# Kernel tuning notes

Measured on AMD Instinct MI355X. Metric: run time of the kernel, lower is better.

The kernel has to match this reference:

```python
import jax, jax.numpy as jnp
import numpy as np

NT, NRV, NR = 100000, 200000, 300000  # tile / road_vertex / road node counts
E = 400000                             # edges per edge type
B, H, P, A = 64, 128, 64, 512          # graphs, hidden, player_state_dim, action_dim


def _gat(h_src, h_dst, src, dst, W, a_s, a_d, b, n_dst):
    # PyG GATConv, heads=1, shared lin for src/dst, no self loops (bipartite)
    hs = h_src @ W                      # [Ns, H]
    hd = h_dst @ W                      # [Nd, H]
    e = jax.nn.leaky_relu((hs @ a_s)[src] + (hd @ a_d)[dst], 0.2)  # [E]
    m = jax.ops.segment_max(e, dst, num_segments=n_dst)
    w = jnp.exp(e - m[dst])
    denom = jax.ops.segment_sum(w, dst, num_segments=n_dst)
    alpha = w / jnp.maximum(denom[dst], 1e-16)                      # segment softmax
    out = jax.ops.segment_sum(alpha[:, None] * hs[src], dst, num_segments=n_dst)
    return out + b


def _mean_pool(x, batch, nb):
    s = jax.ops.segment_sum(x, batch, num_segments=nb)
    c = jax.ops.segment_sum(jnp.ones((x.shape[0],), x.dtype), batch, num_segments=nb)
    return s / jnp.maximum(c, 1.0)[:, None]


def setup_inputs():
    ks = iter(jax.random.split(jax.random.key(0), 64))
    f32 = jnp.float32

    def lin(i, o):
        return (jax.random.normal(next(ks), (i, o), f32) / np.float32(np.sqrt(i)))

    d = {}
    d['x_tile'] = jax.random.normal(next(ks), (NT, 8), f32)
    d['x_rv'] = jax.random.normal(next(ks), (NRV, 13), f32)
    d['x_road'] = jax.random.normal(next(ks), (NR, 4), f32)
    d['x_player'] = jax.random.normal(next(ks), (B, P), f32)
    # node encoders
    d['enc_t_W'] = lin(8, H);  d['enc_t_b'] = jnp.zeros((H,), f32)
    d['enc_rv_W'] = lin(13, H); d['enc_rv_b'] = jnp.zeros((H,), f32)
    d['enc_r_W'] = lin(4, H);  d['enc_r_b'] = jnp.zeros((H,), f32)
    # six GAT convs
    for name in ['rv2t', 't2rv', 'r2rv', 'rv2r', 't2r', 'r2t']:
        d[name + '_W'] = lin(H, H)
        d[name + '_as'] = jax.random.normal(next(ks), (H,), f32) * 0.1
        d[name + '_ad'] = jax.random.normal(next(ks), (H,), f32) * 0.1
        d[name + '_b'] = jnp.zeros((H,), f32)
    # player MLP + output head (input: 3H pooled + H player)
    d['fc1_W'] = lin(P, H); d['fc1_b'] = jnp.zeros((H,), f32)
    d['fc2_W'] = lin(H, H); d['fc2_b'] = jnp.zeros((H,), f32)
    d['out_W'] = lin(4 * H, A); d['out_b'] = jnp.zeros((A,), f32)
    # edges (src bounded by source-type count, dst by dest-type count)
    ri = lambda n, hi: jax.random.randint(n, (E,), 0, hi, jnp.int32)
    d['e_rv2t_src'] = ri(next(ks), NRV); d['e_rv2t_dst'] = ri(next(ks), NT)
    d['e_t2rv_src'] = ri(next(ks), NT);  d['e_t2rv_dst'] = ri(next(ks), NRV)
    d['e_r2rv_src'] = ri(next(ks), NR);  d['e_r2rv_dst'] = ri(next(ks), NRV)
    d['e_rv2r_src'] = ri(next(ks), NRV); d['e_rv2r_dst'] = ri(next(ks), NR)
    d['e_t2r_src'] = ri(next(ks), NT);   d['e_t2r_dst'] = ri(next(ks), NR)
    d['e_r2t_src'] = ri(next(ks), NR);   d['e_r2t_dst'] = ri(next(ks), NT)
    # batch assignment per node type
    d['batch_tile'] = jnp.sort(jax.random.randint(next(ks), (NT,), 0, B, jnp.int32))
    d['batch_rv'] = jnp.sort(jax.random.randint(next(ks), (NRV,), 0, B, jnp.int32))
    d['batch_road'] = jnp.sort(jax.random.randint(next(ks), (NR,), 0, B, jnp.int32))
    return d


def reference(x_tile, x_rv, x_road, x_player,
              enc_t_W, enc_t_b, enc_rv_W, enc_rv_b, enc_r_W, enc_r_b,
              rv2t_W, rv2t_as, rv2t_ad, rv2t_b,
              t2rv_W, t2rv_as, t2rv_ad, t2rv_b,
              r2rv_W, r2rv_as, r2rv_ad, r2rv_b,
              rv2r_W, rv2r_as, rv2r_ad, rv2r_b,
              t2r_W, t2r_as, t2r_ad, t2r_b,
              r2t_W, r2t_as, r2t_ad, r2t_b,
              fc1_W, fc1_b, fc2_W, fc2_b, out_W, out_b,
              e_rv2t_src, e_rv2t_dst, e_t2rv_src, e_t2rv_dst,
              e_r2rv_src, e_r2rv_dst, e_rv2r_src, e_rv2r_dst,
              e_t2r_src, e_t2r_dst, e_r2t_src, e_r2t_dst,
              batch_tile, batch_rv, batch_road):
    # node encoders
    h_t = x_tile @ enc_t_W + enc_t_b
    h_rv = x_rv @ enc_rv_W + enc_rv_b
    h_r = x_road @ enc_r_W + enc_r_b
    # hetero GAT, aggr='sum' over edge types per destination node type
    o_t = (_gat(h_rv, h_t, e_rv2t_src, e_rv2t_dst, rv2t_W, rv2t_as, rv2t_ad, rv2t_b, NT)
           + _gat(h_r, h_t, e_r2t_src, e_r2t_dst, r2t_W, r2t_as, r2t_ad, r2t_b, NT))
    o_rv = (_gat(h_t, h_rv, e_t2rv_src, e_t2rv_dst, t2rv_W, t2rv_as, t2rv_ad, t2rv_b, NRV)
            + _gat(h_r, h_rv, e_r2rv_src, e_r2rv_dst, r2rv_W, r2rv_as, r2rv_ad, r2rv_b, NRV))
    o_r = (_gat(h_rv, h_r, e_rv2r_src, e_rv2r_dst, rv2r_W, rv2r_as, rv2r_ad, rv2r_b, NR)
           + _gat(h_t, h_r, e_t2r_src, e_t2r_dst, t2r_W, t2r_as, t2r_ad, t2r_b, NR))
    # global mean pool per node type, concat -> [B, 3H]
    x_all = jnp.concatenate([_mean_pool(o_t, batch_tile, B),
                             _mean_pool(o_rv, batch_rv, B),
                             _mean_pool(o_r, batch_road, B)], axis=1)
    # player branch
    p = jax.nn.relu(x_player @ fc1_W + fc1_b)
    p = jax.nn.relu(p @ fc2_W + fc2_b)
    x = jnp.concatenate([x_all, p], axis=1)  # [B, 4H]
    return x @ out_W + out_b                 # [B, A]
```

## Files before the change

kernel.cpp:

```cpp
#include <hip/hip_runtime.h>


constexpr int kNT = 100000, kNRV = 200000, kNR = 300000, kE = 400000;
constexpr int kSLOT = 1088;
constexpr int kPSZ  = 6 * kSLOT;
constexpr int kNBE  = 342;
constexpr int kNTH  = kNBE * 256;
constexpr int kEPT  = 5;

constexpr long long OFF_C    = 0;
constexpr long long OFF_VS   = 13056;
constexpr long long OFF_VD   = 13176;
constexpr long long OFF_P8   = 13296;
constexpr long long OFF_LS6  = 65520;
constexpr long long OFF_SRV  = 665520;
constexpr long long OFF_ST   = 3865520;
constexpr long long OFF_SR   = 4665520;
constexpr long long OFF_LDD  = 5865520;

__constant__ const int kDRB[6]  = {0, 100000, 300000, 500000, 800000, 1100000};
__constant__ const int kDLEN[6] = {100000, 200000, 200000, 300000, 300000, 100000};
__constant__ const int kLSB6[6] = {0, 400000, 0, 200000, 500000, 0};

__device__ __forceinline__ int lowb(const int* a, int n, int v) {
  int lo = 0, hi = n;
  while (lo < hi) { int mid = (lo + hi) >> 1; if (a[mid] < v) lo = mid + 1; else hi = mid; }
  return lo;
}

static __device__ __forceinline__ unsigned p2h(float a, float b) {
  _Float16 ha = (_Float16)a, hb = (_Float16)b;
  unsigned short ua = __builtin_bit_cast(unsigned short, ha);
  unsigned short ub = __builtin_bit_cast(unsigned short, hb);
  return (unsigned)ua | ((unsigned)ub << 16);
}

static __device__ __forceinline__ float emb(float ld, int b) {
  return __uint_as_float((__float_as_uint(ld) & ~63u) | (unsigned)b);
}

__global__ __launch_bounds__(256) void precompute_kernel(
    const float* encW_t, const float* encb_t,
    const float* encW_rv, const float* encb_rv,
    const float* encW_r, const float* encb_r,
    const float* W0, const float* as0, const float* ad0,
    const float* W1, const float* as1, const float* ad1,
    const float* W2, const float* as2, const float* ad2,
    const float* W3, const float* as3, const float* ad3,
    const float* W4, const float* as4, const float* ad4,
    const float* W5, const float* as5, const float* ad5,
    float* Cws, float* vsw, float* vdw, float* P8)
{
  const float* encW[3] = {encW_t, encW_rv, encW_r};
  const float* encb[3] = {encb_t, encb_rv, encb_r};
  const int    Ks[3]   = {8, 13, 4};
  const float* Wv[6]  = {W0, W1, W2, W3, W4, W5};
  const float* asv[6] = {as0, as1, as2, as3, as4, as5};
  const float* adv[6] = {ad0, ad1, ad2, ad3, ad4, ad5};
  const int srcT[6] = {1, 0, 2, 1, 0, 2};
  const int dstT[6] = {0, 1, 1, 2, 2, 0};

  __shared__ float Cl[2176];
  __shared__ float wv[128];

  int et = blockIdx.x;
  int tid = threadIdx.x;
  int st = srcT[et], dt = dstT[et];
  const float* eW = encW[st];
  const float* eB = encb[st];
  int K = Ks[st];
  const float* W = Wv[et];
  const float* a_s = asv[et];
  const float* a_d = adv[et];
  float* Cslot = Cws + et * 2176;

  for (int i = et * 256 + tid; i < 8 * kPSZ; i += 6 * 256) P8[i] = 0.f;

  for (int idx = tid; idx < (K + 1) * 128; idx += 256) {
    int r = idx >> 7, j = idx & 127;
    const float* row = (r < K) ? (eW + r * 128) : eB;
    float acc = 0.f;
    for (int m = 0; m < 128; ++m) acc += row[m] * W[m * 128 + j];
    int o = (r < K) ? (r * 128 + j) : (2048 + j);
    Cl[o] = acc;
    Cslot[o] = acc;
  }
  if (tid < 128) {
    float acc = 0.f;
    for (int j = 0; j < 128; ++j) acc += W[tid * 128 + j] * a_d[j];
    wv[tid] = acc;
  }
  __syncthreads();
  if (tid <= K) {
    const float* row = (tid < K) ? (Cl + tid * 128) : (Cl + 2048);
    float acc = 0.f;
    for (int j = 0; j < 128; ++j) acc += row[j] * a_s[j];
    vsw[et * 20 + (tid < K ? tid : 16)] = acc;
  }
  int KD = Ks[dt];
  if (tid >= 32 && tid <= 32 + KD) {
    int k = tid - 32;
    const float* row = (k < KD) ? (encW[dt] + k * 128) : encb[dt];
    float acc = 0.f;
    for (int m = 0; m < 128; ++m) acc += row[m] * wv[m];
    vdw[et * 20 + (k < KD ? k : 16)] = acc;
  }
}

__global__ __launch_bounds__(256) void prep_kernel(
    const float* __restrict__ x_t, const float* __restrict__ x_rv,
    const float* __restrict__ x_r,
    const int* __restrict__ bt, const int* __restrict__ brv,
    const int* __restrict__ br,
    const float* __restrict__ vsw, const float* __restrict__ vdw,
    uint4* __restrict__ SRVq, uint4* __restrict__ STq, uint4* __restrict__ SRq,
    float* __restrict__ LS6, float* __restrict__ LDDf)
{
  int n = blockIdx.x * 256 + threadIdx.x;
  if (n >= kNT + kNRV + kNR) return;
  if (n < kNT) {
    const float* xr = x_t + n * 8;
    int b = bt[n];
    const float* vsA = vsw + 1 * 20, *vsB = vsw + 4 * 20;
    const float* vdA = vdw + 0 * 20, *vdB = vdw + 5 * 20;
    float x[8]; float a0 = 0, a1 = 0, a2 = 0, a3 = 0;
#pragma unroll
    for (int k = 0; k < 8; ++k) {
      x[k] = xr[k];
      a0 += x[k] * vsA[k]; a1 += x[k] * vsB[k];
      a2 += x[k] * vdA[k]; a3 += x[k] * vdB[k];
    }
    float ls1 = a0 + vsA[16], ls4 = a1 + vsB[16];
    float ld0 = a2 + vdA[16], ld5 = a3 + vdB[16];
    STq[(long long)n * 2] =
        make_uint4(p2h(x[0], x[1]), p2h(x[2], x[3]), p2h(x[4], x[5]), p2h(x[6], x[7]));
    STq[(long long)n * 2 + 1] =
        make_uint4(__float_as_uint(ls1), __float_as_uint(ls4), 0, 0);
    LS6[400000 + n] = ls1;
    LS6[500000 + n] = ls4;
    LDDf[(long long)n * 2] = emb(ld0, b);
    LDDf[(long long)n * 2 + 1] = 0.f;
    LDDf[(long long)(1100000 + n) * 2] = emb(ld5, b);
    LDDf[(long long)(1100000 + n) * 2 + 1] = 0.f;
  } else if (n < kNT + kNRV) {
    int m = n - kNT;
    const float* xr = x_rv + m * 13;
    int b = brv[m];
    const float* vsA = vsw + 0 * 20, *vsB = vsw + 3 * 20;
    const float* vdA = vdw + 1 * 20, *vdB = vdw + 2 * 20;
    float x[13]; float a0 = 0, a1 = 0, a2 = 0, a3 = 0;
#pragma unroll
    for (int k = 0; k < 13; ++k) {
      x[k] = xr[k];
      a0 += x[k] * vsA[k]; a1 += x[k] * vsB[k];
      a2 += x[k] * vdA[k]; a3 += x[k] * vdB[k];
    }
    float ls0 = a0 + vsA[16], ls3 = a1 + vsB[16];
    float ld1 = a2 + vdA[16], ld2 = a3 + vdB[16];
    SRVq[(long long)m * 4] =
        make_uint4(p2h(x[0], x[1]), p2h(x[2], x[3]), p2h(x[4], x[5]), p2h(x[6], x[7]));
    SRVq[(long long)m * 4 + 1] =
        make_uint4(p2h(x[8], x[9]), p2h(x[10], x[11]), p2h(x[12], 0.f),
                   __float_as_uint(ls0));
    SRVq[(long long)m * 4 + 2] = make_uint4(__float_as_uint(ls3), 0, 0, 0);
    LS6[m] = ls0;
    LS6[200000 + m] = ls3;
    LDDf[(long long)(100000 + m) * 2] = emb(ld1, b);
    LDDf[(long long)(100000 + m) * 2 + 1] = 0.f;
    LDDf[(long long)(300000 + m) * 2] = emb(ld2, b);
    LDDf[(long long)(300000 + m) * 2 + 1] = 0.f;
  } else {
    int m = n - kNT - kNRV;
    const float* xr = x_r + m * 4;
    int b = br[m];
    const float* vsA = vsw + 2 * 20, *vsB = vsw + 5 * 20;
    const float* vdA = vdw + 3 * 20, *vdB = vdw + 4 * 20;
    float x[4]; float a0 = 0, a1 = 0, a2 = 0, a3 = 0;
#pragma unroll
    for (int k = 0; k < 4; ++k) {
      x[k] = xr[k];
      a0 += x[k] * vsA[k]; a1 += x[k] * vsB[k];
      a2 += x[k] * vdA[k]; a3 += x[k] * vdB[k];
    }
    float ls2 = a0 + vsA[16], ls5 = a1 + vsB[16];
    float ld3 = a2 + vdA[16], ld4 = a3 + vdB[16];
    SRq[m] = make_uint4(p2h(x[0], x[1]), p2h(x[2], x[3]),
                        __float_as_uint(ls2), __float_as_uint(ls5));
    LDDf[(long long)(500000 + m) * 2] = emb(ld3, b);
    LDDf[(long long)(500000 + m) * 2 + 1] = 0.f;
    LDDf[(long long)(800000 + m) * 2] = emb(ld4, b);
    LDDf[(long long)(800000 + m) * 2 + 1] = 0.f;
  }
}

__device__ __forceinline__ void pickSD(
    int et,
    const int* s0, const int* s1, const int* s2,
    const int* s3, const int* s4, const int* s5,
    const int* d0, const int* d1, const int* d2,
    const int* d3, const int* d4, const int* d5,
    const int*& sp, const int*& dp)
{
  switch (et) {
    case 0: sp = s0; dp = d0; break;
    case 1: sp = s1; dp = d1; break;
    case 2: sp = s2; dp = d2; break;
    case 3: sp = s3; dp = d3; break;
    case 4: sp = s4; dp = d4; break;
    default: sp = s5; dp = d5; break;
  }
}

__global__ __launch_bounds__(256, 8) void edgeA_kernel(
    const int* s0, const int* s1, const int* s2,
    const int* s3, const int* s4, const int* s5,
    const int* d0, const int* d1, const int* d2,
    const int* d3, const int* d4, const int* d5,
    const unsigned* __restrict__ SRu, const float* __restrict__ LS6,
    float* __restrict__ LDDf)
{
  int et = blockIdx.x / kNBE;
  int bIdx = blockIdx.x - et * kNBE;
  const int* sp; const int* dp;
  pickSD(et, s0, s1, s2, s3, s4, s5, d0, d1, d2, d3, d4, d5, sp, dp);
  const int drb = kDRB[et];
  int base = bIdx * 256 + (int)threadIdx.x;

  int s[kEPT], d[kEPT]; bool ok[kEPT];
#pragma unroll
  for (int j = 0; j < kEPT; ++j) {
    int e = base + j * kNTH;
    ok[j] = e < kE;
    int ee = ok[j] ? e : 0;
    s[j] = sp[ee]; d[j] = dp[ee];
  }
  float ls[kEPT];
  if (et == 2 || et == 5) {
    const int lso = (et == 2) ? 2 : 3;
#pragma unroll
    for (int j = 0; j < kEPT; ++j)
      ls[j] = __uint_as_float(SRu[(long long)s[j] * 4 + lso]);
  } else {
    const float* L = LS6 + kLSB6[et];
#pragma unroll
    for (int j = 0; j < kEPT; ++j) ls[j] = L[s[j]];
  }
  float ld[kEPT];
#pragma unroll
  for (int j = 0; j < kEPT; ++j)
    ld[j] = LDDf[(long long)(drb + d[j]) * 2];
#pragma unroll
  for (int j = 0; j < kEPT; ++j) {
    float t = ls[j] + ld[j];
    t = t > 0.f ? t : 0.2f * t;
    float w = __expf(t);
    if (ok[j]) unsafeAtomicAdd(&LDDf[(long long)(drb + d[j]) * 2 + 1], w);
  }
}

template <int TYPE, int RSEL>
__device__ __forceinline__ void ebflow(
    int bIdx,
    const int* __restrict__ sp, const int* __restrict__ dp,
    const uint4* __restrict__ srq, const float2* __restrict__ LDD2,
    int drb, int dlen, float* lp)
{
  constexpr int K = (TYPE == 0) ? 8 : ((TYPE == 1) ? 13 : 4);
  const int tid = threadIdx.x;
  const int lane = tid & 63;
  int base = bIdx * 256 + tid;

  int s[kEPT], d[kEPT]; bool ok[kEPT];
#pragma unroll
  for (int j = 0; j < kEPT; ++j) {
    int e = base + j * kNTH;
    ok[j] = e < kE;
    int ee = ok[j] ? e : 0;
    s[j] = sp[ee]; d[j] = dp[ee];
  }
  uint4 q0[kEPT], q1[kEPT];
  float lsx[kEPT];
#pragma unroll
  for (int j = 0; j < kEPT; ++j) {
    if (TYPE == 0) {
      q0[j] = srq[(long long)s[j] * 2];
      lsx[j] = __uint_as_float(
          ((const unsigned*)srq)[(long long)s[j] * 8 + (RSEL ? 5 : 4)]);
    } else if (TYPE == 1) {
      q0[j] = srq[(long long)s[j] * 4];
      q1[j] = srq[(long long)s[j] * 4 + 1];
      lsx[j] = RSEL
          ? __uint_as_float(((const unsigned*)srq)[(long long)s[j] * 16 + 8])
          : __uint_as_float(q1[j].w);
    } else {
      q0[j] = srq[s[j]];
      lsx[j] = __uint_as_float(RSEL ? q0[j].w : q0[j].z);
    }
  }
  float2 f2[kEPT];
#pragma unroll
  for (int j = 0; j < kEPT; ++j) f2[j] = LDD2[drb + d[j]];

#pragma unroll
  for (int j = 0; j < kEPT; ++j) {
    if (!ok[j]) continue;
    int b = (int)(__float_as_uint(f2[j].x) & 63u);
    float t = lsx[j] + f2[j].x;
    t = t > 0.f ? t : 0.2f * t;
    float w = __expf(t);
    float alpha = w / fmaxf(f2[j].y, 1e-16f);
    float xv[K];
    if (TYPE == 0) {
      const _Float16* h = (const _Float16*)&q0[j];
#pragma unroll
      for (int k = 0; k < 8; ++k) xv[k] = (float)h[k];
    } else if (TYPE == 1) {
      const _Float16* h = (const _Float16*)&q0[j];
#pragma unroll
      for (int k = 0; k < 8; ++k) xv[k] = (float)h[k];
      const _Float16* h2 = (const _Float16*)&q1[j];
#pragma unroll
      for (int k = 0; k < 5; ++k) xv[8 + k] = (float)h2[k];
    } else {
      const _Float16* h = (const _Float16*)&q0[j];
#pragma unroll
      for (int k = 0; k < 4; ++k) xv[k] = (float)h[k];
    }
#pragma unroll
    for (int k = 0; k < K; ++k) atomicAdd(lp + k * 64 + b, alpha * xv[k]);
  }

  for (int base2 = bIdx * 256 + (tid & ~63); base2 < dlen; base2 += kNTH) {
    int j2 = base2 + lane;
    bool a2 = j2 < dlen;
    float2 r2 = a2 ? LDD2[drb + j2] : make_float2(0.f, 0.f);
    int b2 = a2 ? (int)(__float_as_uint(r2.x) & 63u) : (64 + lane);
    int v = (a2 && r2.y > 0.f) ? 1 : 0;
#pragma unroll
    for (int d2 = 1; d2 < 64; d2 <<= 1) {
      int ob = __shfl_up(b2, d2);
      int ov = __shfl_up(v, d2);
      if (lane >= d2 && ob == b2) v += ov;
    }
    int bn = __shfl_down(b2, 1);
    if (((lane == 63) || (bn != b2)) && v > 0) atomicAdd(lp + 1024 + b2, (float)v);
  }
}

__global__ __launch_bounds__(256, 4) void edgeB_kernel(
    const int* s0, const int* s1, const int* s2,
    const int* s3, const int* s4, const int* s5,
    const int* d0, const int* d1, const int* d2,
    const int* d3, const int* d4, const int* d5,
    const uint4* SRVq, const uint4* STq, const uint4* SRq,
    const float2* __restrict__ LDD2, float* __restrict__ P8)
{
  __shared__ float lp[kSLOT];
  for (int j = threadIdx.x; j < kSLOT; j += 256) lp[j] = 0.f;
  __syncthreads();
  int et = blockIdx.x / kNBE;
  int bIdx = blockIdx.x - et * kNBE;
  constexpr int KK[6] = {13, 8, 4, 13, 8, 4};
  switch (et) {
    case 0: ebflow<1, 0>(bIdx, s0, d0, SRVq, LDD2, 0,       100000, lp); break;
    case 1: ebflow<0, 0>(bIdx, s1, d1, STq,  LDD2, 100000,  200000, lp); break;
    case 2: ebflow<2, 0>(bIdx, s2, d2, SRq,  LDD2, 300000,  200000, lp); break;
    case 3: ebflow<1, 1>(bIdx, s3, d3, SRVq, LDD2, 500000,  300000, lp); break;
    case 4: ebflow<0, 1>(bIdx, s4, d4, STq,  LDD2, 800000,  300000, lp); break;
    default: ebflow<2, 1>(bIdx, s5, d5, SRq, LDD2, 1100000, 100000, lp); break;
  }
  __syncthreads();
  int K = KK[et];
  float* slab = P8 + (long long)(blockIdx.x & 7) * kPSZ + (long long)et * kSLOT;
  for (int i = threadIdx.x; i < kSLOT; i += 256) {
    if (i >= K * 64 && i < 1024) continue;
    float v = lp[i];
    if (v != 0.f) unsafeAtomicAdd(&slab[i], v);
  }
}

__global__ __launch_bounds__(128) void tail_kernel(
    const int* __restrict__ bt, const int* __restrict__ brv, const int* __restrict__ br,
    const float* __restrict__ xp,
    const float* __restrict__ fc1W, const float* __restrict__ fc1b,
    const float* __restrict__ fc2W, const float* __restrict__ fc2b,
    const float* __restrict__ outW, const float* __restrict__ outb,
    const float* __restrict__ b_rv2t, const float* __restrict__ b_r2t,
    const float* __restrict__ b_t2rv, const float* __restrict__ b_r2rv,
    const float* __restrict__ b_rv2r, const float* __restrict__ b_t2r,
    const float* __restrict__ Cws, const float* __restrict__ P8,
    float* __restrict__ out)
{
  int b = blockIdx.x, tid = threadIdx.x;
  __shared__ float xrow[512];
  __shared__ float p1s[128];
  __shared__ float xps[64];
  __shared__ float psA[15], psB[15];
  __shared__ int cnts[3];

  if (tid < 64) xps[tid] = xp[b * 64 + tid];
  if (tid >= 64 && tid < 67) {
    int t = tid - 64;
    const int* ba = (t == 0) ? bt : (t == 1 ? brv : br);
    int N = (t == 0) ? kNT : (t == 1 ? kNRV : kNR);
    cnts[t] = lowb(ba, N, b + 1) - lowb(ba, N, b);
  }
  __syncthreads();

  float a = fc1b[tid];
  for (int k = 0; k < 64; ++k) a += xps[k] * fc1W[k * 128 + tid];
  p1s[tid] = fmaxf(a, 0.f);
  __syncthreads();
  float a2 = fc2b[tid];
  for (int k = 0; k < 128; ++k) a2 += p1s[k] * fc2W[k * 128 + tid];
  xrow[384 + tid] = fmaxf(a2, 0.f);

  const int etA[3] = {0, 1, 3}, etB[3] = {5, 2, 4};
  const int KAv[3] = {13, 8, 13}, KBv[3] = {4, 4, 8};
  for (int t3 = 0; t3 < 3; ++t3) {
    __syncthreads();
    int eA = etA[t3], eB = etB[t3];
    if (tid < 15) {
      int idx = (tid < 14) ? (tid * 64 + b) : (1024 + b);
      float sum = 0.f;
#pragma unroll
      for (int c = 0; c < 8; ++c) sum += P8[c * kPSZ + eA * kSLOT + idx];
      psA[tid] = sum;
    } else if (tid < 30) {
      int t = tid - 15;
      int idx = (t < 14) ? (t * 64 + b) : (1024 + b);
      float sum = 0.f;
#pragma unroll
      for (int c = 0; c < 8; ++c) sum += P8[c * kPSZ + eB * kSLOT + idx];
      psB[t] = sum;
    }
    __syncthreads();
    int KA = KAv[t3], KB = KBv[t3];
    const float* CA = Cws + eA * 2176;
    const float* CB = Cws + eB * 2176;
    float v = psA[14] * CA[2048 + tid] + psB[14] * CB[2048 + tid];
    for (int k = 0; k < KA; ++k) v += psA[k] * CA[k * 128 + tid];
    for (int k = 0; k < KB; ++k) v += psB[k] * CB[k * 128 + tid];
    float cnt = (float)max(cnts[t3], 1);
    const float* bb1 = (t3 == 0) ? b_rv2t : (t3 == 1 ? b_t2rv : b_rv2r);
    const float* bb2 = (t3 == 0) ? b_r2t  : (t3 == 1 ? b_r2rv : b_t2r);
    xrow[t3 * 128 + tid] = v / cnt + bb1[tid] + bb2[tid];
  }
  __syncthreads();

#pragma unroll
  for (int q = 0; q < 4; ++q) {
    int c = q * 128 + tid;
    float acc = outb[c];
#pragma unroll 8
    for (int k = 0; k < 512; ++k) acc += xrow[k] * outW[k * 512 + c];
    out[b * 512 + c] = acc;
  }
}

extern "C" void kernel_launch(void* const* d_in, const int* in_sizes, int n_in,
                              void* d_out, int out_size, void* d_ws, size_t ws_size,
                              hipStream_t stream) {
  const float* x_tile   = (const float*)d_in[0];
  const float* x_rv     = (const float*)d_in[1];
  const float* x_road   = (const float*)d_in[2];
  const float* x_player = (const float*)d_in[3];
  const float* enc_t_W  = (const float*)d_in[4];
  const float* enc_t_b  = (const float*)d_in[5];
  const float* enc_rv_W = (const float*)d_in[6];
  const float* enc_rv_b = (const float*)d_in[7];
  const float* enc_r_W  = (const float*)d_in[8];
  const float* enc_r_b  = (const float*)d_in[9];
  const float* W[6]; const float* As[6]; const float* Ad[6]; const float* Bb[6];
  for (int et = 0; et < 6; ++et) {
    W[et]  = (const float*)d_in[10 + 4 * et];
    As[et] = (const float*)d_in[11 + 4 * et];
    Ad[et] = (const float*)d_in[12 + 4 * et];
    Bb[et] = (const float*)d_in[13 + 4 * et];
  }
  const float* fc1W = (const float*)d_in[34];
  const float* fc1b = (const float*)d_in[35];
  const float* fc2W = (const float*)d_in[36];
  const float* fc2b = (const float*)d_in[37];
  const float* outW = (const float*)d_in[38];
  const float* outb = (const float*)d_in[39];
  const int* esrc[6]; const int* edst[6];
  for (int et = 0; et < 6; ++et) {
    esrc[et] = (const int*)d_in[40 + 2 * et];
    edst[et] = (const int*)d_in[41 + 2 * et];
  }
  const int* batch_t  = (const int*)d_in[52];
  const int* batch_rv = (const int*)d_in[53];
  const int* batch_r  = (const int*)d_in[54];

  float* wsF = (float*)d_ws;
  float* Cws  = wsF + OFF_C;
  float* vsw  = wsF + OFF_VS;
  float* vdw  = wsF + OFF_VD;
  float* P8   = wsF + OFF_P8;
  float* LS6  = wsF + OFF_LS6;
  uint4* SRVq = (uint4*)(wsF + OFF_SRV);
  uint4* STq  = (uint4*)(wsF + OFF_ST);
  uint4* SRq  = (uint4*)(wsF + OFF_SR);
  float* LDDf = wsF + OFF_LDD;
  float2* LDD2 = (float2*)(wsF + OFF_LDD);
  float* out  = (float*)d_out;

  precompute_kernel<<<6, 256, 0, stream>>>(
      enc_t_W, enc_t_b, enc_rv_W, enc_rv_b, enc_r_W, enc_r_b,
      W[0], As[0], Ad[0], W[1], As[1], Ad[1], W[2], As[2], Ad[2],
      W[3], As[3], Ad[3], W[4], As[4], Ad[4], W[5], As[5], Ad[5],
      Cws, vsw, vdw, P8);

  prep_kernel<<<(kNT + kNRV + kNR + 255) / 256, 256, 0, stream>>>(
      x_tile, x_rv, x_road, batch_t, batch_rv, batch_r, vsw, vdw,
      SRVq, STq, SRq, LS6, LDDf);

  edgeA_kernel<<<6 * kNBE, 256, 0, stream>>>(
      esrc[0], esrc[1], esrc[2], esrc[3], esrc[4], esrc[5],
      edst[0], edst[1], edst[2], edst[3], edst[4], edst[5],
      (const unsigned*)SRq, LS6, LDDf);

  edgeB_kernel<<<6 * kNBE, 256, 0, stream>>>(
      esrc[0], esrc[1], esrc[2], esrc[3], esrc[4], esrc[5],
      edst[0], edst[1], edst[2], edst[3], edst[4], edst[5],
      SRVq, STq, SRq, LDD2, P8);

  tail_kernel<<<64, 128, 0, stream>>>(
      batch_t, batch_rv, batch_r, x_player,
      fc1W, fc1b, fc2W, fc2b, outW, outb,
      Bb[0], Bb[5], Bb[1], Bb[2], Bb[3], Bb[4],
      Cws, P8, out);

  (void)in_sizes; (void)n_in; (void)out_size; (void)ws_size;
}
```

Baseline: 598.0 us.

## Store per-edge fp16 softmax weights in pass A and shrink node records

Pass A now writes each edge's exp weight as fp16 into a per-edge buffer, and pass B reads it instead of re-gathering the source logit and recomputing the exponential. Node records get smaller: source logits move out of the packed feature records, destination logits go to a separate array, and the denominator is paired with the graph id stored as a float. Partial-sum slabs drop from 8 to 4, which cuts the tail reduction but adds more atomic contention. The cost is an extra 2-byte write and read per edge, plus fp16 rounding of the attention weights.

```diff
diff --git a/kernel.cpp b/kernel.cpp
--- a/kernel.cpp
+++ b/kernel.cpp
@@ -11,16 +11,18 @@
 constexpr long long OFF_C    = 0;
 constexpr long long OFF_VS   = 13056;
 constexpr long long OFF_VD   = 13176;
-constexpr long long OFF_P8   = 13296;
-constexpr long long OFF_LS6  = 65520;
-constexpr long long OFF_SRV  = 665520;
-constexpr long long OFF_ST   = 3865520;
-constexpr long long OFF_SR   = 4665520;
-constexpr long long OFF_LDD  = 5865520;
+constexpr long long OFF_P4   = 13296;
+constexpr long long OFF_LS6  = 39408;
+constexpr long long OFF_LD6  = 1239408;
+constexpr long long OFF_W16  = 2439408;
+constexpr long long OFF_DEN  = 3639408;
+constexpr long long OFF_SRV  = 6039408;
+constexpr long long OFF_ST   = 7639408;
+constexpr long long OFF_SR   = 8039408;
 
 __constant__ const int kDRB[6]  = {0, 100000, 300000, 500000, 800000, 1100000};
 __constant__ const int kDLEN[6] = {100000, 200000, 200000, 300000, 300000, 100000};
-__constant__ const int kLSB6[6] = {0, 400000, 0, 200000, 500000, 0};
+__constant__ const int kLSB6[6] = {0, 400000, 600000, 200000, 500000, 900000};
 
 __device__ __forceinline__ int lowb(const int* a, int n, int v) {
   int lo = 0, hi = n;
@@ -33,10 +35,6 @@
   unsigned short ua = __builtin_bit_cast(unsigned short, ha);
   unsigned short ub = __builtin_bit_cast(unsigned short, hb);
   return (unsigned)ua | ((unsigned)ub << 16);
-}
-
-static __device__ __forceinline__ float emb(float ld, int b) {
-  return __uint_as_float((__float_as_uint(ld) & ~63u) | (unsigned)b);
 }
 
 __global__ __launch_bounds__(256) void precompute_kernel(
@@ -49,7 +47,7 @@
     const float* W3, const float* as3, const float* ad3,
     const float* W4, const float* as4, const float* ad4,
     const float* W5, const float* as5, const float* ad5,
-    float* Cws, float* vsw, float* vdw, float* P8)
+    float* Cws, float* vsw, float* vdw, float* P4)
 {
   const float* encW[3] = {encW_t, encW_rv, encW_r};
   const float* encb[3] = {encb_t, encb_rv, encb_r};
@@ -74,7 +72,7 @@
   const float* a_d = adv[et];
   float* Cslot = Cws + et * 2176;
 
-  for (int i = et * 256 + tid; i < 8 * kPSZ; i += 6 * 256) P8[i] = 0.f;
+  for (int i = et * 256 + tid; i < 4 * kPSZ; i += 6 * 256) P4[i] = 0.f;
 
   for (int idx = tid; idx < (K + 1) * 128; idx += 256) {
     int r = idx >> 7, j = idx & 127;
@@ -113,14 +111,15 @@
     const int* __restrict__ bt, const int* __restrict__ brv,
     const int* __restrict__ br,
     const float* __restrict__ vsw, const float* __restrict__ vdw,
-    uint4* __restrict__ SRVq, uint4* __restrict__ STq, uint4* __restrict__ SRq,
-    float* __restrict__ LS6, float* __restrict__ LDDf)
+    uint4* __restrict__ SRVq, uint4* __restrict__ STq, uint2* __restrict__ SRq,
+    float* __restrict__ LS6, float* __restrict__ LD6,
+    float2* __restrict__ DEN)
 {
   int n = blockIdx.x * 256 + threadIdx.x;
   if (n >= kNT + kNRV + kNR) return;
   if (n < kNT) {
     const float* xr = x_t + n * 8;
-    int b = bt[n];
+    float bf = (float)bt[n];
     const float* vsA = vsw + 1 * 20, *vsB = vsw + 4 * 20;
     const float* vdA = vdw + 0 * 20, *vdB = vdw + 5 * 20;
     float x[8]; float a0 = 0, a1 = 0, a2 = 0, a3 = 0;
@@ -130,22 +129,18 @@
       a0 += x[k] * vsA[k]; a1 += x[k] * vsB[k];
       a2 += x[k] * vdA[k]; a3 += x[k] * vdB[k];
     }
-    float ls1 = a0 + vsA[16], ls4 = a1 + vsB[16];
-    float ld0 = a2 + vdA[16], ld5 = a3 + vdB[16];
-    STq[(long long)n * 2] =
-        make_uint4(p2h(x[0], x[1]), p2h(x[2], x[3]), p2h(x[4], x[5]), p2h(x[6], x[7]));
-    STq[(long long)n * 2 + 1] =
-        make_uint4(__float_as_uint(ls1), __float_as_uint(ls4), 0, 0);
-    LS6[400000 + n] = ls1;
-    LS6[500000 + n] = ls4;
-    LDDf[(long long)n * 2] = emb(ld0, b);
-    LDDf[(long long)n * 2 + 1] = 0.f;
-    LDDf[(long long)(1100000 + n) * 2] = emb(ld5, b);
-    LDDf[(long long)(1100000 + n) * 2 + 1] = 0.f;
+    STq[n] = make_uint4(p2h(x[0], x[1]), p2h(x[2], x[3]),
+                        p2h(x[4], x[5]), p2h(x[6], x[7]));
+    LS6[400000 + n] = a0 + vsA[16];
+    LS6[500000 + n] = a1 + vsB[16];
+    LD6[n] = a2 + vdA[16];
+    LD6[1100000 + n] = a3 + vdB[16];
+    DEN[n] = make_float2(0.f, bf);
+    DEN[1100000 + n] = make_float2(0.f, bf);
   } else if (n < kNT + kNRV) {
     int m = n - kNT;
     const float* xr = x_rv + m * 13;
-    int b = brv[m];
+    float bf = (float)brv[m];
     const float* vsA = vsw + 0 * 20, *vsB = vsw + 3 * 20;
     const float* vdA = vdw + 1 * 20, *vdB = vdw + 2 * 20;
     float x[13]; float a0 = 0, a1 = 0, a2 = 0, a3 = 0;
@@ -155,24 +150,20 @@
       a0 += x[k] * vsA[k]; a1 += x[k] * vsB[k];
       a2 += x[k] * vdA[k]; a3 += x[k] * vdB[k];
     }
-    float ls0 = a0 + vsA[16], ls3 = a1 + vsB[16];
-    float ld1 = a2 + vdA[16], ld2 = a3 + vdB[16];
-    SRVq[(long long)m * 4] =
+    SRVq[(long long)m * 2] =
         make_uint4(p2h(x[0], x[1]), p2h(x[2], x[3]), p2h(x[4], x[5]), p2h(x[6], x[7]));
-    SRVq[(long long)m * 4 + 1] =
-        make_uint4(p2h(x[8], x[9]), p2h(x[10], x[11]), p2h(x[12], 0.f),
-                   __float_as_uint(ls0));
-    SRVq[(long long)m * 4 + 2] = make_uint4(__float_as_uint(ls3), 0, 0, 0);
-    LS6[m] = ls0;
-    LS6[200000 + m] = ls3;
-    LDDf[(long long)(100000 + m) * 2] = emb(ld1, b);
-    LDDf[(long long)(100000 + m) * 2 + 1] = 0.f;
-    LDDf[(long long)(300000 + m) * 2] = emb(ld2, b);
-    LDDf[(long long)(300000 + m) * 2 + 1] = 0.f;
+    SRVq[(long long)m * 2 + 1] =
+        make_uint4(p2h(x[8], x[9]), p2h(x[10], x[11]), p2h(x[12], 0.f), 0);
+    LS6[m] = a0 + vsA[16];
+    LS6[200000 + m] = a1 + vsB[16];
+    LD6[100000 + m] = a2 + vdA[16];
+    LD6[300000 + m] = a3 + vdB[16];
+    DEN[100000 + m] = make_float2(0.f, bf);
+    DEN[300000 + m] = make_float2(0.f, bf);
   } else {
     int m = n - kNT - kNRV;
     const float* xr = x_r + m * 4;
-    int b = br[m];
+    float bf = (float)br[m];
     const float* vsA = vsw + 2 * 20, *vsB = vsw + 5 * 20;
     const float* vdA = vdw + 3 * 20, *vdB = vdw + 4 * 20;
     float x[4]; float a0 = 0, a1 = 0, a2 = 0, a3 = 0;
@@ -182,14 +173,13 @@
       a0 += x[k] * vsA[k]; a1 += x[k] * vsB[k];
       a2 += x[k] * vdA[k]; a3 += x[k] * vdB[k];
     }
-    float ls2 = a0 + vsA[16], ls5 = a1 + vsB[16];
-    float ld3 = a2 + vdA[16], ld4 = a3 + vdB[16];
-    SRq[m] = make_uint4(p2h(x[0], x[1]), p2h(x[2], x[3]),
-                        __float_as_uint(ls2), __float_as_uint(ls5));
-    LDDf[(long long)(500000 + m) * 2] = emb(ld3, b);
-    LDDf[(long long)(500000 + m) * 2 + 1] = 0.f;
-    LDDf[(long long)(800000 + m) * 2] = emb(ld4, b);
-    LDDf[(long long)(800000 + m) * 2 + 1] = 0.f;
+    SRq[m] = make_uint2(p2h(x[0], x[1]), p2h(x[2], x[3]));
+    LS6[600000 + m] = a0 + vsA[16];
+    LS6[900000 + m] = a1 + vsB[16];
+    LD6[500000 + m] = a2 + vdA[16];
+    LD6[800000 + m] = a3 + vdB[16];
+    DEN[500000 + m] = make_float2(0.f, bf);
+    DEN[800000 + m] = make_float2(0.f, bf);
   }
 }
 
@@ -216,14 +206,17 @@
     const int* s3, const int* s4, const int* s5,
     const int* d0, const int* d1, const int* d2,
     const int* d3, const int* d4, const int* d5,
-    const unsigned* __restrict__ SRu, const float* __restrict__ LS6,
-    float* __restrict__ LDDf)
+    const float* __restrict__ LS6, const float* __restrict__ LD6,
+    _Float16* __restrict__ W16, float* __restrict__ DENf)
 {
   int et = blockIdx.x / kNBE;
   int bIdx = blockIdx.x - et * kNBE;
   const int* sp; const int* dp;
   pickSD(et, s0, s1, s2, s3, s4, s5, d0, d1, d2, d3, d4, d5, sp, dp);
+  const float* Lsrc = LS6 + kLSB6[et];
+  const float* Ldst = LD6 + kDRB[et];
   const int drb = kDRB[et];
+  _Float16* Wet = W16 + (long long)et * kE;
   int base = bIdx * 256 + (int)threadIdx.x;
 
   int s[kEPT], d[kEPT]; bool ok[kEPT];
@@ -235,34 +228,29 @@
     s[j] = sp[ee]; d[j] = dp[ee];
   }
   float ls[kEPT];
-  if (et == 2 || et == 5) {
-    const int lso = (et == 2) ? 2 : 3;
-#pragma unroll
-    for (int j = 0; j < kEPT; ++j)
-      ls[j] = __uint_as_float(SRu[(long long)s[j] * 4 + lso]);
-  } else {
-    const float* L = LS6 + kLSB6[et];
-#pragma unroll
-    for (int j = 0; j < kEPT; ++j) ls[j] = L[s[j]];
-  }
+#pragma unroll
+  for (int j = 0; j < kEPT; ++j) ls[j] = Lsrc[s[j]];
   float ld[kEPT];
 #pragma unroll
-  for (int j = 0; j < kEPT; ++j)
-    ld[j] = LDDf[(long long)(drb + d[j]) * 2];
+  for (int j = 0; j < kEPT; ++j) ld[j] = Ldst[d[j]];
 #pragma unroll
   for (int j = 0; j < kEPT; ++j) {
     float t = ls[j] + ld[j];
     t = t > 0.f ? t : 0.2f * t;
     float w = __expf(t);
-    if (ok[j]) unsafeAtomicAdd(&LDDf[(long long)(drb + d[j]) * 2 + 1], w);
-  }
-}
-
-template <int TYPE, int RSEL>
+    if (ok[j]) {
+      Wet[base + j * kNTH] = (_Float16)w;
+      unsafeAtomicAdd(&DENf[(long long)(drb + d[j]) * 2], w);
+    }
+  }
+}
+
+template <int TYPE>
 __device__ __forceinline__ void ebflow(
     int bIdx,
     const int* __restrict__ sp, const int* __restrict__ dp,
-    const uint4* __restrict__ srq, const float2* __restrict__ LDD2,
+    const uint4* __restrict__ srq4, const uint2* __restrict__ srq2,
+    const _Float16* __restrict__ Wet, const float2* __restrict__ DEN2,
     int drb, int dlen, float* lp)
 {
   constexpr int K = (TYPE == 0) ? 8 : ((TYPE == 1) ? 13 : 4);
@@ -278,37 +266,33 @@
     int ee = ok[j] ? e : 0;
     s[j] = sp[ee]; d[j] = dp[ee];
   }
-  uint4 q0[kEPT], q1[kEPT];
-  float lsx[kEPT];
+  float w[kEPT];
+#pragma unroll
+  for (int j = 0; j < kEPT; ++j) {
+    int e = base + j * kNTH;
+    w[j] = (float)Wet[ok[j] ? e : 0];
+  }
+  uint4 q0[kEPT], q1[kEPT]; uint2 r2v[kEPT];
 #pragma unroll
   for (int j = 0; j < kEPT; ++j) {
     if (TYPE == 0) {
-      q0[j] = srq[(long long)s[j] * 2];
-      lsx[j] = __uint_as_float(
-          ((const unsigned*)srq)[(long long)s[j] * 8 + (RSEL ? 5 : 4)]);
+      q0[j] = srq4[s[j]];
     } else if (TYPE == 1) {
-      q0[j] = srq[(long long)s[j] * 4];
-      q1[j] = srq[(long long)s[j] * 4 + 1];
-      lsx[j] = RSEL
-          ? __uint_as_float(((const unsigned*)srq)[(long long)s[j] * 16 + 8])
-          : __uint_as_float(q1[j].w);
+      q0[j] = srq4[(long long)s[j] * 2];
+      q1[j] = srq4[(long long)s[j] * 2 + 1];
     } else {
-      q0[j] = srq[s[j]];
-      lsx[j] = __uint_as_float(RSEL ? q0[j].w : q0[j].z);
+      r2v[j] = srq2[s[j]];
     }
   }
   float2 f2[kEPT];
 #pragma unroll
-  for (int j = 0; j < kEPT; ++j) f2[j] = LDD2[drb + d[j]];
+  for (int j = 0; j < kEPT; ++j) f2[j] = DEN2[drb + d[j]];
 
 #pragma unroll
   for (int j = 0; j < kEPT; ++j) {
     if (!ok[j]) continue;
-    int b = (int)(__float_as_uint(f2[j].x) & 63u);
-    float t = lsx[j] + f2[j].x;
-    t = t > 0.f ? t : 0.2f * t;
-    float w = __expf(t);
-    float alpha = w / fmaxf(f2[j].y, 1e-16f);
+    int b = (int)f2[j].y;
+    float alpha = w[j] / fmaxf(f2[j].x, 1e-16f);
     float xv[K];
     if (TYPE == 0) {
       const _Float16* h = (const _Float16*)&q0[j];
@@ -322,7 +306,7 @@
 #pragma unroll
       for (int k = 0; k < 5; ++k) xv[8 + k] = (float)h2[k];
     } else {
-      const _Float16* h = (const _Float16*)&q0[j];
+      const _Float16* h = (const _Float16*)&r2v[j];
 #pragma unroll
       for (int k = 0; k < 4; ++k) xv[k] = (float)h[k];
     }
@@ -333,9 +317,9 @@
   for (int base2 = bIdx * 256 + (tid & ~63); base2 < dlen; base2 += kNTH) {
     int j2 = base2 + lane;
     bool a2 = j2 < dlen;
-    float2 r2 = a2 ? LDD2[drb + j2] : make_float2(0.f, 0.f);
-    int b2 = a2 ? (int)(__float_as_uint(r2.x) & 63u) : (64 + lane);
-    int v = (a2 && r2.y > 0.f) ? 1 : 0;
+    float2 r2 = a2 ? DEN2[drb + j2] : make_float2(0.f, 0.f);
+    int b2 = a2 ? (int)r2.y : (64 + lane);
+    int v = (a2 && r2.x > 0.f) ? 1 : 0;
 #pragma unroll
     for (int d2 = 1; d2 < 64; d2 <<= 1) {
       int ob = __shfl_up(b2, d2);
@@ -352,26 +336,28 @@
     const int* s3, const int* s4, const int* s5,
     const int* d0, const int* d1, const int* d2,
     const int* d3, const int* d4, const int* d5,
-    const uint4* SRVq, const uint4* STq, const uint4* SRq,
-    const float2* __restrict__ LDD2, float* __restrict__ P8)
+    const uint4* SRVq, const uint4* STq, const uint2* SRq,
+    const _Float16* __restrict__ W16, const float2* __restrict__ DEN2,
+    float* __restrict__ P4)
 {
   __shared__ float lp[kSLOT];
   for (int j = threadIdx.x; j < kSLOT; j += 256) lp[j] = 0.f;
   __syncthreads();
   int et = blockIdx.x / kNBE;
   int bIdx = blockIdx.x - et * kNBE;
+  const _Float16* Wet = W16 + (long long)et * kE;
   constexpr int KK[6] = {13, 8, 4, 13, 8, 4};
   switch (et) {
-    case 0: ebflow<1, 0>(bIdx, s0, d0, SRVq, LDD2, 0,       100000, lp); break;
-    case 1: ebflow<0, 0>(bIdx, s1, d1, STq,  LDD2, 100000,  200000, lp); break;
-    case 2: ebflow<2, 0>(bIdx, s2, d2, SRq,  LDD2, 300000,  200000, lp); break;
-    case 3: ebflow<1, 1>(bIdx, s3, d3, SRVq, LDD2, 500000,  300000, lp); break;
-    case 4: ebflow<0, 1>(bIdx, s4, d4, STq,  LDD2, 800000,  300000, lp); break;
-    default: ebflow<2, 1>(bIdx, s5, d5, SRq, LDD2, 1100000, 100000, lp); break;
+    case 0: ebflow<1>(bIdx, s0, d0, SRVq, nullptr, Wet, DEN2, 0,       100000, lp); break;
+    case 1: ebflow<0>(bIdx, s1, d1, STq,  nullptr, Wet, DEN2, 100000,  200000, lp); break;
+    case 2: ebflow<2>(bIdx, s2, d2, nullptr, SRq,  Wet, DEN2, 300000,  200000, lp); break;
+    case 3: ebflow<1>(bIdx, s3, d3, SRVq, nullptr, Wet, DEN2, 500000,  300000, lp); break;
+    case 4: ebflow<0>(bIdx, s4, d4, STq,  nullptr, Wet, DEN2, 800000,  300000, lp); break;
+    default: ebflow<2>(bIdx, s5, d5, nullptr, SRq, Wet, DEN2, 1100000, 100000, lp); break;
   }
   __syncthreads();
   int K = KK[et];
-  float* slab = P8 + (long long)(blockIdx.x & 7) * kPSZ + (long long)et * kSLOT;
+  float* slab = P4 + (long long)(blockIdx.x & 3) * kPSZ + (long long)et * kSLOT;
   for (int i = threadIdx.x; i < kSLOT; i += 256) {
     if (i >= K * 64 && i < 1024) continue;
     float v = lp[i];
@@ -388,7 +374,7 @@
     const float* __restrict__ b_rv2t, const float* __restrict__ b_r2t,
     const float* __restrict__ b_t2rv, const float* __restrict__ b_r2rv,
     const float* __restrict__ b_rv2r, const float* __restrict__ b_t2r,
-    const float* __restrict__ Cws, const float* __restrict__ P8,
+    const float* __restrict__ Cws, const float* __restrict__ P4,
     float* __restrict__ out)
 {
   int b = blockIdx.x, tid = threadIdx.x;
@@ -424,14 +410,14 @@
       int idx = (tid < 14) ? (tid * 64 + b) : (1024 + b);
       float sum = 0.f;
 #pragma unroll
-      for (int c = 0; c < 8; ++c) sum += P8[c * kPSZ + eA * kSLOT + idx];
+      for (int c = 0; c < 4; ++c) sum += P4[c * kPSZ + eA * kSLOT + idx];
       psA[tid] = sum;
     } else if (tid < 30) {
       int t = tid - 15;
       int idx = (t < 14) ? (t * 64 + b) : (1024 + b);
       float sum = 0.f;
 #pragma unroll
-      for (int c = 0; c < 8; ++c) sum += P8[c * kPSZ + eB * kSLOT + idx];
+      for (int c = 0; c < 4; ++c) sum += P4[c * kPSZ + eB * kSLOT + idx];
       psB[t] = sum;
     }
     __syncthreads();
@@ -497,40 +483,42 @@
   float* Cws  = wsF + OFF_C;
   float* vsw  = wsF + OFF_VS;
   float* vdw  = wsF + OFF_VD;
-  float* P8   = wsF + OFF_P8;
+  float* P4   = wsF + OFF_P4;
   float* LS6  = wsF + OFF_LS6;
+  float* LD6  = wsF + OFF_LD6;
+  _Float16* W16 = (_Float16*)(wsF + OFF_W16);
+  float* DENf = wsF + OFF_DEN;
+  float2* DEN2 = (float2*)(wsF + OFF_DEN);
   uint4* SRVq = (uint4*)(wsF + OFF_SRV);
   uint4* STq  = (uint4*)(wsF + OFF_ST);
-  uint4* SRq  = (uint4*)(wsF + OFF_SR);
-  float* LDDf = wsF + OFF_LDD;
-  float2* LDD2 = (float2*)(wsF + OFF_LDD);
+  uint2* SRq  = (uint2*)(wsF + OFF_SR);
   float* out  = (float*)d_out;
 
   precompute_kernel<<<6, 256, 0, stream>>>(
       enc_t_W, enc_t_b, enc_rv_W, enc_rv_b, enc_r_W, enc_r_b,
       W[0], As[0], Ad[0], W[1], As[1], Ad[1], W[2], As[2], Ad[2],
       W[3], As[3], Ad[3], W[4], As[4], Ad[4], W[5], As[5], Ad[5],
-      Cws, vsw, vdw, P8);
+      Cws, vsw, vdw, P4);
 
   prep_kernel<<<(kNT + kNRV + kNR + 255) / 256, 256, 0, stream>>>(
       x_tile, x_rv, x_road, batch_t, batch_rv, batch_r, vsw, vdw,
-      SRVq, STq, SRq, LS6, LDDf);
+      SRVq, STq, SRq, LS6, LD6, DEN2);
 
   edgeA_kernel<<<6 * kNBE, 256, 0, stream>>>(
       esrc[0], esrc[1], esrc[2], esrc[3], esrc[4], esrc[5],
       edst[0], edst[1], edst[2], edst[3], edst[4], edst[5],
-      (const unsigned*)SRq, LS6, LDDf);
+      LS6, LD6, W16, DENf);
 
   edgeB_kernel<<<6 * kNBE, 256, 0, stream>>>(
       esrc[0], esrc[1], esrc[2], esrc[3], esrc[4], esrc[5],
       edst[0], edst[1], edst[2], edst[3], edst[4], edst[5],
-      SRVq, STq, SRq, LDD2, P8);
+      SRVq, STq, SRq, W16, DEN2, P4);
 
   tail_kernel<<<64, 128, 0, stream>>>(
       batch_t, batch_rv, batch_r, x_player,
       fc1W, fc1b, fc2W, fc2b, outW, outb,
       Bb[0], Bb[5], Bb[1], Bb[2], Bb[3], Bb[4],
-      Cws, P8, out);
+      Cws, P4, out);
 
   (void)in_sizes; (void)n_in; (void)out_size; (void)ws_size;
 }
```

After: 579.1 us. -3.2%, faster.
